# Kernel tuning notes

Hardware: AMD Instinct MI355X
Metric: run time of the kernel (lower is better)

Reference implementation:

```python
import jax, jax.numpy as jnp
import numpy as np

ALPHA = 0.2  # LeakyReLU negative slope
NEG_INF = -9e15


def setup_inputs() -> dict:
    key = jax.random.key(0)
    k1, k2, k3, k4 = jax.random.split(key, 4)
    N, F_in, F_out = 8192, 128, 64
    x = jax.random.normal(k1, (N, F_in), dtype=jnp.float32)
    adj = jax.random.randint(k2, (N, N), 0, 2, dtype=jnp.int32)
    W = jax.random.normal(k3, (F_in, F_out), dtype=jnp.float32) * 0.1
    a = jax.random.normal(k4, (2 * F_out, 1), dtype=jnp.float32) * 0.1
    return {"x": x, "adj": adj, "W": W, "a": a}


def reference(x, adj, W, a):
    F_out = W.shape[1]
    Wh = x @ W                         # [N, F_out]
    Wh1 = Wh @ a[:F_out, :]            # [N, 1]
    Wh2 = Wh @ a[F_out:, :]            # [N, 1]
    e = Wh1 + Wh2.T                    # [N, N] broadcast scores
    e = jnp.where(e > 0, e, ALPHA * e) # LeakyReLU
    e = jnp.where(adj > 0, e, NEG_INF) # mask non-edges
    attention = jax.nn.softmax(e, axis=1)
    out = attention @ Wh               # [N, F_out]
    return jax.nn.elu(out)             # concat=True -> ELU
```

## Files before the change

kernel.cpp:

```cpp
#include <hip/hip_runtime.h>
#include <hip/hip_bf16.h>

#define NN 8192
#define FIN 128
#define FOUT 64
#define ALPHA 0.2f
#define CHUNK 256
#define BM 16
#define NCHUNK (NN / CHUNK)
#define PROW (CHUNK + 8)

typedef __attribute__((ext_vector_type(8))) short short8;
typedef __attribute__((ext_vector_type(4))) float floatx4;

static __device__ __forceinline__ ushort f2bf(float f) {
    __hip_bfloat16 h = __float2bfloat16(f);
    return __builtin_bit_cast(ushort, h);
}

__global__ __launch_bounds__(256) void gat_proj(const float* __restrict__ x,
                                                const float* __restrict__ W,
                                                const float* __restrict__ a,
                                                ushort* __restrict__ WhT,
                                                float* __restrict__ Wh1,
                                                float* __restrict__ Wh2) {
    const int t = threadIdx.x;
    const int f = t & 63;
    const int rl = t >> 6;
    const int row = blockIdx.x * 4 + rl;
    const float4* __restrict__ x4 = (const float4*)(x + (size_t)row * FIN);

    float acc = 0.f;
    #pragma unroll
    for (int k4 = 0; k4 < FIN / 4; ++k4) {
        float4 xv = x4[k4];
        const int k = k4 * 4;
        acc = fmaf(xv.x, W[(k + 0) * FOUT + f], acc);
        acc = fmaf(xv.y, W[(k + 1) * FOUT + f], acc);
        acc = fmaf(xv.z, W[(k + 2) * FOUT + f], acc);
        acc = fmaf(xv.w, W[(k + 3) * FOUT + f], acc);
    }
    WhT[(size_t)f * NN + row] = f2bf(acc);

    float s1 = acc * a[f];
    float s2 = acc * a[FOUT + f];
    #pragma unroll
    for (int off = 32; off; off >>= 1) {
        s1 += __shfl_xor(s1, off, 64);
        s2 += __shfl_xor(s2, off, 64);
    }
    if (f == 0) { Wh1[row] = s1; Wh2[row] = s2; }
}

__global__ __launch_bounds__(256) void gat_attn(const int* __restrict__ adj,
                                                const ushort* __restrict__ WhT,
                                                const float* __restrict__ Wh1,
                                                const float* __restrict__ Wh2,
                                                float* __restrict__ out) {
    __shared__ __align__(16) ushort P[2][BM][PROW];
    __shared__ float denL[BM];

    const int t = threadIdx.x;
    const int lane = t & 63;
    const int wv = t >> 6;
    const int row0 = blockIdx.x * BM;
    const int ln = lane & 15;
    const int quad = lane >> 4;

    const float4 wh1v = *(const float4*)(Wh1 + row0 + wv * 4);
    const int* __restrict__ aptr = adj + (size_t)(row0 + wv * 4) * NN + lane * 4;

    floatx4 acc = {0.f, 0.f, 0.f, 0.f};
    float den0 = 0.f, den1 = 0.f, den2 = 0.f, den3 = 0.f;

    auto computeP = [&](int c, int b) {
        const int jb = c * CHUNK;
        const float4 wh2v = *(const float4*)(Wh2 + jb + lane * 4);
        const int4 av0 = *(const int4*)(aptr + (size_t)0 * NN + jb);
        const int4 av1 = *(const int4*)(aptr + (size_t)1 * NN + jb);
        const int4 av2 = *(const int4*)(aptr + (size_t)2 * NN + jb);
        const int4 av3 = *(const int4*)(aptr + (size_t)3 * NN + jb);
#define ROWP(AV, W1, DEN, II)                                              \
        {                                                                  \
            float s0 = (W1) + wh2v.x, s1 = (W1) + wh2v.y,                  \
                  s2 = (W1) + wh2v.z, s3 = (W1) + wh2v.w;                  \
            s0 = fmaxf(s0, ALPHA * s0); s1 = fmaxf(s1, ALPHA * s1);        \
            s2 = fmaxf(s2, ALPHA * s2); s3 = fmaxf(s3, ALPHA * s3);        \
            float p0 = __expf(s0), p1 = __expf(s1),                        \
                  p2 = __expf(s2), p3 = __expf(s3);                        \
            p0 = (AV.x > 0) ? p0 : 0.f; p1 = (AV.y > 0) ? p1 : 0.f;        \
            p2 = (AV.z > 0) ? p2 : 0.f; p3 = (AV.w > 0) ? p3 : 0.f;       \
            DEN += (p0 + p1) + (p2 + p3);                                  \
            ushort4 pk = make_ushort4(f2bf(p0), f2bf(p1), f2bf(p2), f2bf(p3)); \
            *(ushort4*)&P[b][wv * 4 + (II)][lane * 4] = pk;                \
        }
        ROWP(av0, wh1v.x, den0, 0)
        ROWP(av1, wh1v.y, den1, 1)
        ROWP(av2, wh1v.z, den2, 2)
        ROWP(av3, wh1v.w, den3, 3)
#undef ROWP
    };

    computeP(0, 0);
    __syncthreads();

    int pb = 0;
    for (int c = 0; c < NCHUNK; ++c) {
        if (c + 1 < NCHUNK) computeP(c + 1, pb ^ 1);

        const int jb = c * CHUNK;
        const ushort* Arow = &P[pb][ln][quad * 8];
        const ushort* Brow = WhT + (size_t)(wv * 16 + ln) * NN + jb + quad * 8;
        #pragma unroll
        for (int k0 = 0; k0 < 8; ++k0) {
            short8 af = *(const short8*)(Arow + k0 * 32);
            short8 bf = *(const short8*)(Brow + k0 * 32);
            acc = __builtin_amdgcn_mfma_f32_16x16x32_bf16(af, bf, acc, 0, 0, 0);
        }
        __syncthreads();
        pb ^= 1;
    }

    float dsum[4] = {den0, den1, den2, den3};
    #pragma unroll
    for (int ii = 0; ii < 4; ++ii) {
        float d = dsum[ii];
        #pragma unroll
        for (int off = 32; off; off >>= 1) d += __shfl_xor(d, off, 64);
        if (lane == 0) denL[wv * 4 + ii] = d;
    }
    __syncthreads();

    #pragma unroll
    for (int r = 0; r < 4; ++r) {
        const int i = quad * 4 + r;
        float o = acc[r] / denL[i];
        o = (o > 0.f) ? o : (__expf(o) - 1.f);
        out[(size_t)(row0 + i) * FOUT + wv * 16 + ln] = o;
    }
}

extern "C" void kernel_launch(void* const* d_in, const int* in_sizes, int n_in,
                              void* d_out, int out_size, void* d_ws, size_t ws_size,
                              hipStream_t stream) {
    const float* x   = (const float*)d_in[0];
    const int*   adj = (const int*)  d_in[1];
    const float* W   = (const float*)d_in[2];
    const float* a   = (const float*)d_in[3];
    float* out = (float*)d_out;

    ushort* WhT = (ushort*)d_ws;
    float* Wh1 = (float*)(WhT + (size_t)FOUT * NN);
    float* Wh2 = Wh1 + NN;

    gat_proj<<<NN / 4, 256, 0, stream>>>(x, W, a, WhT, Wh1, Wh2);
    gat_attn<<<NN / BM, 256, 0, stream>>>(adj, WhT, Wh1, Wh2, out);
}
```

Before: 399.6 us.

## Compute attention probabilities in registers as MFMA A operands with split-K waves

Each wave now handles a slice of the key dimension for all 16 rows and all 64 output features. It computes the masked exp scores directly into MFMA A-fragment registers instead of staging them through a double-buffered LDS tile, so the per-chunk __syncthreads go away. Wh2 is preloaded into 32KB of shared memory and the adjacency loads are software-pipelined across two register sets. Partial accumulators and denominators from the four waves are reduced through LDS at the end; the larger LDS footprint may lower occupancy.

```diff
diff --git a/kernel.cpp b/kernel.cpp
--- a/kernel.cpp
+++ b/kernel.cpp
@@ -5,10 +5,7 @@
 #define FIN 128
 #define FOUT 64
 #define ALPHA 0.2f
-#define CHUNK 256
-#define BM 16
-#define NCHUNK (NN / CHUNK)
-#define PROW (CHUNK + 8)
+#define NCH 32
 
 typedef __attribute__((ext_vector_type(8))) short short8;
 typedef __attribute__((ext_vector_type(4))) float floatx4;
@@ -57,86 +54,129 @@
                                                 const float* __restrict__ Wh1,
                                                 const float* __restrict__ Wh2,
                                                 float* __restrict__ out) {
-    __shared__ __align__(16) ushort P[2][BM][PROW];
-    __shared__ float denL[BM];
+    __shared__ __align__(16) float sWh2[NN];
+    __shared__ float sAcc[4][4][16][16];
+    __shared__ float sDen[4][16];
 
     const int t = threadIdx.x;
     const int lane = t & 63;
     const int wv = t >> 6;
-    const int row0 = blockIdx.x * BM;
     const int ln = lane & 15;
     const int quad = lane >> 4;
+    const int row0 = blockIdx.x * 16;
 
-    const float4 wh1v = *(const float4*)(Wh1 + row0 + wv * 4);
-    const int* __restrict__ aptr = adj + (size_t)(row0 + wv * 4) * NN + lane * 4;
+    {
+        const float4* __restrict__ s = (const float4*)Wh2;
+        float4* d = (float4*)sWh2;
+        #pragma unroll
+        for (int i = 0; i < 8; ++i) d[i * 256 + t] = s[i * 256 + t];
+    }
 
-    floatx4 acc = {0.f, 0.f, 0.f, 0.f};
-    float den0 = 0.f, den1 = 0.f, den2 = 0.f, den3 = 0.f;
+    const float wh1 = Wh1[row0 + ln];
+    const int4* __restrict__ ap =
+        (const int4*)(adj + (size_t)(row0 + ln) * NN) + (wv * 16 + quad * 2);
+    const ushort* __restrict__ bp = WhT + (size_t)ln * NN + wv * 64 + quad * 8;
+    const float4* __restrict__ sW2v = (const float4*)sWh2;
+    const int jq = wv * 16 + quad * 2;
 
-    auto computeP = [&](int c, int b) {
-        const int jb = c * CHUNK;
-        const float4 wh2v = *(const float4*)(Wh2 + jb + lane * 4);
-        const int4 av0 = *(const int4*)(aptr + (size_t)0 * NN + jb);
-        const int4 av1 = *(const int4*)(aptr + (size_t)1 * NN + jb);
-        const int4 av2 = *(const int4*)(aptr + (size_t)2 * NN + jb);
-        const int4 av3 = *(const int4*)(aptr + (size_t)3 * NN + jb);
-#define ROWP(AV, W1, DEN, II)                                              \
-        {                                                                  \
-            float s0 = (W1) + wh2v.x, s1 = (W1) + wh2v.y,                  \
-                  s2 = (W1) + wh2v.z, s3 = (W1) + wh2v.w;                  \
-            s0 = fmaxf(s0, ALPHA * s0); s1 = fmaxf(s1, ALPHA * s1);        \
-            s2 = fmaxf(s2, ALPHA * s2); s3 = fmaxf(s3, ALPHA * s3);        \
-            float p0 = __expf(s0), p1 = __expf(s1),                        \
-                  p2 = __expf(s2), p3 = __expf(s3);                        \
-            p0 = (AV.x > 0) ? p0 : 0.f; p1 = (AV.y > 0) ? p1 : 0.f;        \
-            p2 = (AV.z > 0) ? p2 : 0.f; p3 = (AV.w > 0) ? p3 : 0.f;       \
-            DEN += (p0 + p1) + (p2 + p3);                                  \
-            ushort4 pk = make_ushort4(f2bf(p0), f2bf(p1), f2bf(p2), f2bf(p3)); \
-            *(ushort4*)&P[b][wv * 4 + (II)][lane * 4] = pk;                \
-        }
-        ROWP(av0, wh1v.x, den0, 0)
-        ROWP(av1, wh1v.y, den1, 1)
-        ROWP(av2, wh1v.z, den2, 2)
-        ROWP(av3, wh1v.w, den3, 3)
-#undef ROWP
-    };
+    floatx4 acc0 = {0.f, 0.f, 0.f, 0.f};
+    floatx4 acc1 = {0.f, 0.f, 0.f, 0.f};
+    floatx4 acc2 = {0.f, 0.f, 0.f, 0.f};
+    floatx4 acc3 = {0.f, 0.f, 0.f, 0.f};
+    float den = 0.f;
 
-    computeP(0, 0);
     __syncthreads();
 
-    int pb = 0;
-    for (int c = 0; c < NCHUNK; ++c) {
-        if (c + 1 < NCHUNK) computeP(c + 1, pb ^ 1);
+#define LOADADJ(L0, H0, L1, H1, C) {                                         \
+    L0 = ap[(C) * 64];                                                       \
+    H0 = ap[(C) * 64 + 1];                                                   \
+    L1 = ap[(C) * 64 + 8];                                                   \
+    H1 = ap[(C) * 64 + 9];                                                   \
+}
 
-        const int jb = c * CHUNK;
-        const ushort* Arow = &P[pb][ln][quad * 8];
-        const ushort* Brow = WhT + (size_t)(wv * 16 + ln) * NN + jb + quad * 8;
-        #pragma unroll
-        for (int k0 = 0; k0 < 8; ++k0) {
-            short8 af = *(const short8*)(Arow + k0 * 32);
-            short8 bf = *(const short8*)(Brow + k0 * 32);
-            acc = __builtin_amdgcn_mfma_f32_16x16x32_bf16(af, bf, acc, 0, 0, 0);
-        }
-        __syncthreads();
-        pb ^= 1;
+#define SCORE8(LO, HI, C, KS, AF) {                                          \
+    float4 wa = sW2v[(C) * 64 + (KS) * 8 + jq];                              \
+    float4 wb = sW2v[(C) * 64 + (KS) * 8 + jq + 1];                          \
+    float s0 = wh1 + wa.x, s1 = wh1 + wa.y, s2 = wh1 + wa.z, s3 = wh1 + wa.w;\
+    float s4 = wh1 + wb.x, s5 = wh1 + wb.y, s6 = wh1 + wb.z, s7 = wh1 + wb.w;\
+    s0 = fmaxf(s0, ALPHA * s0); s1 = fmaxf(s1, ALPHA * s1);                  \
+    s2 = fmaxf(s2, ALPHA * s2); s3 = fmaxf(s3, ALPHA * s3);                  \
+    s4 = fmaxf(s4, ALPHA * s4); s5 = fmaxf(s5, ALPHA * s5);                  \
+    s6 = fmaxf(s6, ALPHA * s6); s7 = fmaxf(s7, ALPHA * s7);                  \
+    float p0 = (LO.x > 0) ? __expf(s0) : 0.f;                                \
+    float p1 = (LO.y > 0) ? __expf(s1) : 0.f;                                \
+    float p2 = (LO.z > 0) ? __expf(s2) : 0.f;                                \
+    float p3 = (LO.w > 0) ? __expf(s3) : 0.f;                                \
+    float p4 = (HI.x > 0) ? __expf(s4) : 0.f;                                \
+    float p5 = (HI.y > 0) ? __expf(s5) : 0.f;                                \
+    float p6 = (HI.z > 0) ? __expf(s6) : 0.f;                                \
+    float p7 = (HI.w > 0) ? __expf(s7) : 0.f;                                \
+    den += ((p0 + p1) + (p2 + p3)) + ((p4 + p5) + (p6 + p7));                \
+    AF[0] = (short)f2bf(p0); AF[1] = (short)f2bf(p1);                        \
+    AF[2] = (short)f2bf(p2); AF[3] = (short)f2bf(p3);                        \
+    AF[4] = (short)f2bf(p4); AF[5] = (short)f2bf(p5);                        \
+    AF[6] = (short)f2bf(p6); AF[7] = (short)f2bf(p7);                        \
+}
+
+#define BODY(L0, H0, L1, H1, C) {                                            \
+    const ushort* bq = bp + (size_t)(C) * 256;                               \
+    short8 b00 = *(const short8*)(bq);                                       \
+    short8 b01 = *(const short8*)(bq + (size_t)16 * NN);                     \
+    short8 b02 = *(const short8*)(bq + (size_t)32 * NN);                     \
+    short8 b03 = *(const short8*)(bq + (size_t)48 * NN);                     \
+    short8 b10 = *(const short8*)(bq + 32);                                  \
+    short8 b11 = *(const short8*)(bq + (size_t)16 * NN + 32);                \
+    short8 b12 = *(const short8*)(bq + (size_t)32 * NN + 32);                \
+    short8 b13 = *(const short8*)(bq + (size_t)48 * NN + 32);                \
+    short8 af0, af1;                                                         \
+    SCORE8(L0, H0, C, 0, af0)                                                \
+    SCORE8(L1, H1, C, 1, af1)                                                \
+    acc0 = __builtin_amdgcn_mfma_f32_16x16x32_bf16(af0, b00, acc0, 0, 0, 0); \
+    acc1 = __builtin_amdgcn_mfma_f32_16x16x32_bf16(af0, b01, acc1, 0, 0, 0); \
+    acc2 = __builtin_amdgcn_mfma_f32_16x16x32_bf16(af0, b02, acc2, 0, 0, 0); \
+    acc3 = __builtin_amdgcn_mfma_f32_16x16x32_bf16(af0, b03, acc3, 0, 0, 0); \
+    acc0 = __builtin_amdgcn_mfma_f32_16x16x32_bf16(af1, b10, acc0, 0, 0, 0); \
+    acc1 = __builtin_amdgcn_mfma_f32_16x16x32_bf16(af1, b11, acc1, 0, 0, 0); \
+    acc2 = __builtin_amdgcn_mfma_f32_16x16x32_bf16(af1, b12, acc2, 0, 0, 0); \
+    acc3 = __builtin_amdgcn_mfma_f32_16x16x32_bf16(af1, b13, acc3, 0, 0, 0); \
+}
+
+    int4 xl0, xh0, xl1, xh1, yl0, yh0, yl1, yh1;
+    LOADADJ(xl0, xh0, xl1, xh1, 0)
+    for (int c = 0; c < NCH; c += 2) {
+        LOADADJ(yl0, yh0, yl1, yh1, c + 1)
+        BODY(xl0, xh0, xl1, xh1, c)
+        const int c2 = (c + 2 < NCH) ? (c + 2) : 0;
+        LOADADJ(xl0, xh0, xl1, xh1, c2)
+        BODY(yl0, yh0, yl1, yh1, c + 1)
     }
 
-    float dsum[4] = {den0, den1, den2, den3};
+#undef BODY
+#undef SCORE8
+#undef LOADADJ
+
+    den += __shfl_xor(den, 16, 64);
+    den += __shfl_xor(den, 32, 64);
+    if (lane < 16) sDen[wv][lane] = den;
+
     #pragma unroll
-    for (int ii = 0; ii < 4; ++ii) {
-        float d = dsum[ii];
-        #pragma unroll
-        for (int off = 32; off; off >>= 1) d += __shfl_xor(d, off, 64);
-        if (lane == 0) denL[wv * 4 + ii] = d;
+    for (int r = 0; r < 4; ++r) {
+        const int m = quad * 4 + r;
+        sAcc[wv][0][m][ln] = acc0[r];
+        sAcc[wv][1][m][ln] = acc1[r];
+        sAcc[wv][2][m][ln] = acc2[r];
+        sAcc[wv][3][m][ln] = acc3[r];
     }
     __syncthreads();
 
     #pragma unroll
     for (int r = 0; r < 4; ++r) {
-        const int i = quad * 4 + r;
-        float o = acc[r] / denL[i];
+        const int m = quad * 4 + r;
+        float d = sDen[0][m] + sDen[1][m] + sDen[2][m] + sDen[3][m];
+        float o = (sAcc[0][wv][m][ln] + sAcc[1][wv][m][ln] +
+                   sAcc[2][wv][m][ln] + sAcc[3][wv][m][ln]) / d;
         o = (o > 0.f) ? o : (__expf(o) - 1.f);
-        out[(size_t)(row0 + i) * FOUT + wv * 16 + ln] = o;
+        out[(size_t)(row0 + m) * FOUT + wv * 16 + ln] = o;
     }
 }
 
@@ -154,5 +194,5 @@
     float* Wh2 = Wh1 + NN;
 
     gat_proj<<<NN / 4, 256, 0, stream>>>(x, W, a, WhT, Wh1, Wh2);
-    gat_attn<<<NN / BM, 256, 0, stream>>>(adj, WhT, Wh1, Wh2, out);
+    gat_attn<<<NN / 16, 256, 0, stream>>>(adj, WhT, Wh1, Wh2, out);
 }
```

New measurement: 406.0 us. No clear change (+1.6%).
